# Kernel optimization log

Hardware: AMD Instinct MI355X
Metric: run time of the kernel (lower is better)

The kernel has to match this reference:

```python
import jax, jax.numpy as jnp
import numpy as np

BLOCK_H = 32
BLOCK_W = 32
HEADS = 16
SEQ = 1024
BATCH = 8
HEAD_DIM = 64


def _block_mask(mask):
    # conv with all-ones kernel, stride = block size, grouped per head == block sum-pool, then >0
    H, S, Sw = mask.shape
    nb_h, nb_w = S // BLOCK_H, Sw // BLOCK_W
    pooled = mask.reshape(H, nb_h, BLOCK_H, nb_w, BLOCK_W).sum(axis=(2, 4))
    return pooled > 0  # [H, nb_h, nb_w] bool


def setup_inputs() -> dict:
    key = jax.random.key(0)
    kq, kk, kv, km = jax.random.split(key, 4)
    q = jax.random.normal(kq, (BATCH, HEADS, SEQ, HEAD_DIM), dtype=jnp.float32)
    k = jax.random.normal(kk, (BATCH, HEADS, SEQ, HEAD_DIM), dtype=jnp.float32)
    v = jax.random.normal(kv, (BATCH, HEADS, SEQ, HEAD_DIM), dtype=jnp.float32)
    # with diagonal blocks always present (valid causal layout, matches triton usage).
    nb = SEQ // BLOCK_H
    bm = jax.random.uniform(km, (HEADS, nb, nb)) < 0.25
    bm = bm | jnp.eye(nb, dtype=bool)[None, :, :]
    # expand block mask to element-level float mask [H, S, S]
    mask = jnp.broadcast_to(
        bm[:, :, None, :, None], (HEADS, nb, BLOCK_H, nb, BLOCK_W)
    ).reshape(HEADS, SEQ, SEQ).astype(jnp.float32)
    return {"query": q, "key": k, "value": v, "mask": mask}


def reference(query, key, value, mask):
    scale = 1.0
    bm = _block_mask(mask)  # [H, nb, nb]
    nb = bm.shape[-1]
    # expand block layout back to element granularity (triton masks per-block only)
    elem = jnp.broadcast_to(
        bm[:, :, None, :, None], (bm.shape[0], nb, BLOCK_H, nb, BLOCK_W)
    ).reshape(bm.shape[0], nb * BLOCK_H, nb * BLOCK_W)
    causal = jnp.tril(jnp.ones((elem.shape[-2], elem.shape[-1]), dtype=bool))
    full = elem & causal[None]  # [H, S, S]
    # SDD: QK^T only on layout blocks; dense equivalent masks to -inf elsewhere
    scores = jnp.einsum("bhqd,bhkd->bhqk", query, key) * scale
    scores = jnp.where(full[None], scores, -jnp.inf)
    probs = jax.nn.softmax(scores, axis=-1)  # every row has a valid diagonal-block entry
    # DSD: sparse probs @ dense V
    out = jnp.einsum("bhqk,bhkd->bhqd", probs, value)
    return out
```

## Files before the change

### kernel.cpp

```cpp
#include <hip/hip_runtime.h>
#include <stdint.h>

typedef unsigned short u16;
typedef short bf16x8 __attribute__((ext_vector_type(8)));
typedef bf16x8 __attribute__((may_alias)) bf16x8_a;
typedef unsigned u32x2 __attribute__((ext_vector_type(2)));
typedef u32x2 __attribute__((may_alias)) u32x2_a;
typedef float f32x4 __attribute__((ext_vector_type(4)));
typedef f32x4 __attribute__((may_alias)) f32x4_a;

#define BATCH 8
#define HEADS 16
#define SEQ 1024
#define HD 64
#define NB 32
#define LOG2E 1.44269504f
#define MBIAS 46.16624128f
#define BLK 2048

__device__ unsigned g_bm[HEADS * NB];
__device__ u16 g_kb[(size_t)BATCH * HEADS * NB * BLK];
__device__ u16 g_kl[(size_t)BATCH * HEADS * NB * BLK];
__device__ u16 g_vt[(size_t)BATCH * HEADS * NB * BLK];

__device__ __forceinline__ u16 f2bf(float x) {
    unsigned u = __builtin_bit_cast(unsigned, x);
    u += 0x7fffu + ((u >> 16) & 1u);
    return (u16)(u >> 16);
}
__device__ __forceinline__ float bf2f(u16 h) {
    unsigned u = ((unsigned)h) << 16;
    return __builtin_bit_cast(float, u);
}
__device__ __forceinline__ bf16x8 pack8(float4 a, float4 b) {
    bf16x8 r;
    r[0] = (short)f2bf(a.x); r[1] = (short)f2bf(a.y);
    r[2] = (short)f2bf(a.z); r[3] = (short)f2bf(a.w);
    r[4] = (short)f2bf(b.x); r[5] = (short)f2bf(b.y);
    r[6] = (short)f2bf(b.z); r[7] = (short)f2bf(b.w);
    return r;
}
__device__ __forceinline__ bf16x8 pack8_res(float4 a, float4 b, bf16x8 hi) {
    bf16x8 r;
    r[0] = (short)f2bf(a.x - bf2f((u16)hi[0])); r[1] = (short)f2bf(a.y - bf2f((u16)hi[1]));
    r[2] = (short)f2bf(a.z - bf2f((u16)hi[2])); r[3] = (short)f2bf(a.w - bf2f((u16)hi[3]));
    r[4] = (short)f2bf(b.x - bf2f((u16)hi[4])); r[5] = (short)f2bf(b.y - bf2f((u16)hi[5]));
    r[6] = (short)f2bf(b.z - bf2f((u16)hi[6])); r[7] = (short)f2bf(b.w - bf2f((u16)hi[7]));
    return r;
}

__global__ __launch_bounds__(256) void prep_kv(const float* __restrict__ k,
                                               const float* __restrict__ v,
                                               const float* __restrict__ mask) {
    __shared__ float tile[32 * 65];
    int bid = blockIdx.x;
    int t = threadIdx.x;
    if (bid < 4096) {
        int bh = bid >> 5, j = bid & 31;
        int row = t >> 3, dg = t & 7;
        const float* s = k + ((size_t)(bh * SEQ + j * 32 + row)) * HD + dg * 8;
        float4 a = *(const float4*)(s);
        float4 b = *(const float4*)(s + 4);
        bf16x8 hi = pack8(a, b);
        bf16x8 lo = pack8_res(a, b, hi);
        int c = ((row >> 4) << 1) + (dg >> 2);
        int lane = (row & 15) + ((dg & 3) << 4);
        size_t o = ((size_t)(bh * NB + j)) * BLK + c * 512 + lane * 8;
        *(bf16x8*)(g_kb + o) = hi;
        *(bf16x8*)(g_kl + o) = lo;
        return;
    }
    if (bid < 6144) {
        int tb = bid - 4096;
        int bh = tb >> 4, kt = tb & 15;
        const float* src = v + ((size_t)(bh * SEQ + kt * 64)) * HD;
#pragma unroll
        for (int pass = 0; pass < 2; ++pass) {
#pragma unroll
            for (int p = 0; p < 2; ++p) {
                int row = p * 16 + (t >> 4);
                int col = (t & 15) * 4;
                float4 d = *(const float4*)(src + (size_t)(pass * 32 + row) * HD + col);
                float* tp = &tile[row * 65 + col];
                tp[0] = d.x; tp[1] = d.y; tp[2] = d.z; tp[3] = d.w;
            }
            __syncthreads();
            {
                int dd = t >> 2;
                int kc = (t & 3) * 8;
                u16 tmp[8];
#pragma unroll
                for (int i = 0; i < 8; ++i) tmp[i] = f2bf(tile[(kc + i) * 65 + dd]);
                int j = kt * 2 + pass;
                int c = dd >> 4;
                int lane = (dd & 15) + ((kc >> 3) << 4);
                size_t o = ((size_t)(bh * NB + j)) * BLK + c * 512 + lane * 8;
                *(uint4*)(g_vt + o) = *(const uint4*)tmp;
            }
            __syncthreads();
        }
        return;
    }
    int h = bid - 6144;
    int lane = t & 63;
#pragma unroll
    for (int kk2 = 0; kk2 < 4; ++kk2) {
        int tt = (kk2 << 8) | t;
        int i = tt >> 5, j = tt & 31;
        float mv = mask[(size_t)h * SEQ * SEQ + (size_t)(i * 32) * SEQ + (size_t)(j * 32)];
        bool pred = (j == i) || (j < i && mv != 0.0f);
        unsigned long long bal = __ballot(pred);
        if (lane == 0)  g_bm[h * NB + i] = (unsigned)(bal & 0xffffffffull);
        if (lane == 32) g_bm[h * NB + i] = (unsigned)(bal >> 32);
    }
}

__device__ __forceinline__ void load_blk(size_t kb, bf16x8 (&kh)[4], bf16x8 (&kl)[4],
                                         bf16x8 (&vf)[4]) {
#pragma unroll
    for (int c = 0; c < 4; ++c) {
        kh[c] = *(const bf16x8_a*)(const void*)(g_kb + kb + c * 512);
        kl[c] = *(const bf16x8_a*)(const void*)(g_kl + kb + c * 512);
        vf[c] = *(const bf16x8_a*)(const void*)(g_vt + kb + c * 512);
    }
}

__device__ __forceinline__ void compute_blk(int j, int i32, int qcol, int quad,
                                            const bf16x8 (&kh)[4], const bf16x8 (&kl)[4],
                                            const bf16x8 (&vf)[4],
                                            const bf16x8 (&qh)[2][2], const bf16x8 (&ql)[2][2],
                                            u16* pl, f32x4 (&oacc)[2][4], float& l0, float& l1) {
    f32x4 tt[2][2];
    __builtin_amdgcn_s_setprio(1);
#pragma unroll
    for (int kt = 0; kt < 2; ++kt)
#pragma unroll
        for (int t = 0; t < 2; ++t) {
            f32x4 acc = f32x4{0.f, 0.f, 0.f, 0.f};
            acc = __builtin_amdgcn_mfma_f32_16x16x32_bf16(kl[kt*2+0], qh[t][0], acc, 0, 0, 0);
            acc = __builtin_amdgcn_mfma_f32_16x16x32_bf16(kl[kt*2+1], qh[t][1], acc, 0, 0, 0);
            acc = __builtin_amdgcn_mfma_f32_16x16x32_bf16(kh[kt*2+0], ql[t][0], acc, 0, 0, 0);
            acc = __builtin_amdgcn_mfma_f32_16x16x32_bf16(kh[kt*2+1], ql[t][1], acc, 0, 0, 0);
            acc = __builtin_amdgcn_mfma_f32_16x16x32_bf16(kh[kt*2+0], qh[t][0], acc, 0, 0, 0);
            acc = __builtin_amdgcn_mfma_f32_16x16x32_bf16(kh[kt*2+1], qh[t][1], acc, 0, 0, 0);
            tt[kt][t] = acc;
        }
    __builtin_amdgcn_s_setprio(0);

    if (j == i32) {
#pragma unroll
        for (int kt = 0; kt < 2; ++kt)
#pragma unroll
            for (int t = 0; t < 2; ++t)
#pragma unroll
                for (int r = 0; r < 4; ++r) {
                    int key = kt * 16 + quad * 4 + r;
                    if (key > t * 16 + qcol) tt[kt][t][r] = -1e30f;
                }
    }

    u16 pb[2][8];
#pragma unroll
    for (int kt = 0; kt < 2; ++kt)
#pragma unroll
        for (int t = 0; t < 2; ++t) {
            float psum = 0.f;
#pragma unroll
            for (int r = 0; r < 4; ++r) {
                float e = exp2f(tt[kt][t][r] * LOG2E - MBIAS);
                u16 eb = f2bf(e);
                pb[t][kt * 4 + r] = eb;
                psum += bf2f(eb);
            }
            if (t == 0) l0 += psum; else l1 += psum;
        }

#pragma unroll
    for (int t = 0; t < 2; ++t)
#pragma unroll
        for (int kt = 0; kt < 2; ++kt) {
            u32x2 pw;
            pw[0] = (unsigned)pb[t][kt*4+0] | ((unsigned)pb[t][kt*4+1] << 16);
            pw[1] = (unsigned)pb[t][kt*4+2] | ((unsigned)pb[t][kt*4+3] << 16);
            *(u32x2_a*)(pl + (t * 16 + qcol) * 40 + kt * 16 + quad * 4) = pw;
        }
    bf16x8 pf0 = *(const bf16x8_a*)(pl + qcol * 40 + quad * 8);
    bf16x8 pf1 = *(const bf16x8_a*)(pl + (16 + qcol) * 40 + quad * 8);

    __builtin_amdgcn_s_setprio(1);
#pragma unroll
    for (int c = 0; c < 4; ++c) {
        oacc[0][c] = __builtin_amdgcn_mfma_f32_16x16x32_bf16(vf[c], pf0, oacc[0][c], 0, 0, 0);
        oacc[1][c] = __builtin_amdgcn_mfma_f32_16x16x32_bf16(vf[c], pf1, oacc[1][c], 0, 0, 0);
    }
    __builtin_amdgcn_s_setprio(0);
}

__global__ __launch_bounds__(64, 2) void attn(const float* __restrict__ q,
                                              float* __restrict__ out) {
    __shared__ __align__(16) char smem[8704];

    int lane = threadIdx.x & 63;
    int qcol = lane & 15;
    int quad = lane >> 4;

    int bid = blockIdx.x;
    int slot = bid & 7;
    int r = bid >> 3;
    int half = r >> 8;
    int rr = r & 255;
    int i32 = 31 - (rr >> 3);
    int bh = slot + ((((half << 3) | (rr & 7))) << 3);
    int h = bh & (HEADS - 1);

    bf16x8 qh[2][2], ql[2][2];
#pragma unroll
    for (int t = 0; t < 2; ++t) {
        const float* qb = q + ((size_t)(bh * SEQ + i32 * 32 + t * 16 + qcol)) * HD + quad * 8;
#pragma unroll
        for (int dh = 0; dh < 2; ++dh) {
            float4 a = *(const float4*)(qb + dh * 32);
            float4 b = *(const float4*)(qb + dh * 32 + 4);
            qh[t][dh] = pack8(a, b);
            ql[t][dh] = pack8_res(a, b, qh[t][dh]);
        }
    }

    unsigned bits = g_bm[h * NB + i32];
    size_t bhbase = (size_t)bh * NB * BLK + lane * 8;
    u16* pl = (u16*)smem;

    f32x4 oacc[2][4];
#pragma unroll
    for (int t = 0; t < 2; ++t)
#pragma unroll
        for (int c = 0; c < 4; ++c) oacc[t][c] = f32x4{0.f, 0.f, 0.f, 0.f};
    float l0 = 0.f, l1 = 0.f;

    bf16x8 khA[4], klA[4], vfA[4], khB[4], klB[4], vfB[4];
    unsigned rem = bits;
    if (rem) {
        int jA = __builtin_ctz(rem); rem &= rem - 1;
        load_blk(bhbase + (size_t)jA * BLK, khA, klA, vfA);
        for (;;) {
            int jB = -1;
            if (rem) { jB = __builtin_ctz(rem); rem &= rem - 1;
                       load_blk(bhbase + (size_t)jB * BLK, khB, klB, vfB); }
            compute_blk(jA, i32, qcol, quad, khA, klA, vfA, qh, ql, pl, oacc, l0, l1);
            if (jB < 0) break;
            jA = -1;
            if (rem) { jA = __builtin_ctz(rem); rem &= rem - 1;
                       load_blk(bhbase + (size_t)jA * BLK, khA, klA, vfA); }
            compute_blk(jB, i32, qcol, quad, khB, klB, vfB, qh, ql, pl, oacc, l0, l1);
            if (jA < 0) break;
        }
    }

    l0 += __shfl_xor(l0, 16); l0 += __shfl_xor(l0, 32);
    l1 += __shfl_xor(l1, 16); l1 += __shfl_xor(l1, 32);
    float inv[2] = {1.0f / l0, 1.0f / l1};

    float* ol = (float*)smem;
#pragma unroll
    for (int t = 0; t < 2; ++t)
#pragma unroll
        for (int c = 0; c < 4; ++c) {
            f32x4 val;
            val[0] = oacc[t][c][0] * inv[t]; val[1] = oacc[t][c][1] * inv[t];
            val[2] = oacc[t][c][2] * inv[t]; val[3] = oacc[t][c][3] * inv[t];
            *(f32x4_a*)(ol + (t * 16 + qcol) * 68 + c * 16 + quad * 4) = val;
        }
    float* obase = out + ((size_t)(bh * SEQ + i32 * 32)) * HD;
#pragma unroll
    for (int gr = 0; gr < 8; ++gr) {
        int row = gr * 4 + (lane >> 4);
        int colf = (lane & 15) * 4;
        f32x4 val = *(const f32x4_a*)(ol + row * 68 + colf);
        *(float4*)(obase + (size_t)row * HD + colf) = make_float4(val[0], val[1], val[2], val[3]);
    }
}

extern "C" void kernel_launch(void* const* d_in, const int* in_sizes, int n_in,
                              void* d_out, int out_size, void* d_ws, size_t ws_size,
                              hipStream_t stream) {
    const float* q = (const float*)d_in[0];
    const float* k = (const float*)d_in[1];
    const float* v = (const float*)d_in[2];
    const float* mask = (const float*)d_in[3];
    float* out = (float*)d_out;

    prep_kv<<<4096 + 2048 + 16, 256, 0, stream>>>(k, v, mask);
    attn<<<4096, 64, 0, stream>>>(q, out);
}
```

Before: 200.4 us.

## Split query block across two waves with shared LDS-staged K/V double buffer

The attention kernel now uses two waves per block, each owning 16 query rows, instead of one wave handling all 32 rows. K-hi, K-lo and V^T tiles are copied into a double-buffered LDS stage with global_load_lds, split between the waves, so both waves share one copy of each key block. The next block's copy is issued before the current one is computed. This cuts per-wave register pressure and duplicate global loads, and it writes output directly from registers. In exchange it adds a __syncthreads and a full vmcnt wait on every iteration.

```diff
diff --git a/kernel.cpp b/kernel.cpp
--- a/kernel.cpp
+++ b/kernel.cpp
@@ -47,6 +47,12 @@
     r[4] = (short)f2bf(b.x - bf2f((u16)hi[4])); r[5] = (short)f2bf(b.y - bf2f((u16)hi[5]));
     r[6] = (short)f2bf(b.z - bf2f((u16)hi[6])); r[7] = (short)f2bf(b.w - bf2f((u16)hi[7]));
     return r;
+}
+
+__device__ __forceinline__ void cp16(u16* lds_uniform, const u16* g_perlane) {
+    __builtin_amdgcn_global_load_lds(
+        (const __attribute__((address_space(1))) unsigned int*)g_perlane,
+        (__attribute__((address_space(3))) unsigned int*)lds_uniform, 16, 0, 0);
 }
 
 __global__ __launch_bounds__(256) void prep_kv(const float* __restrict__ k,
@@ -115,91 +121,12 @@
     }
 }
 
-__device__ __forceinline__ void load_blk(size_t kb, bf16x8 (&kh)[4], bf16x8 (&kl)[4],
-                                         bf16x8 (&vf)[4]) {
-#pragma unroll
-    for (int c = 0; c < 4; ++c) {
-        kh[c] = *(const bf16x8_a*)(const void*)(g_kb + kb + c * 512);
-        kl[c] = *(const bf16x8_a*)(const void*)(g_kl + kb + c * 512);
-        vf[c] = *(const bf16x8_a*)(const void*)(g_vt + kb + c * 512);
-    }
-}
-
-__device__ __forceinline__ void compute_blk(int j, int i32, int qcol, int quad,
-                                            const bf16x8 (&kh)[4], const bf16x8 (&kl)[4],
-                                            const bf16x8 (&vf)[4],
-                                            const bf16x8 (&qh)[2][2], const bf16x8 (&ql)[2][2],
-                                            u16* pl, f32x4 (&oacc)[2][4], float& l0, float& l1) {
-    f32x4 tt[2][2];
-    __builtin_amdgcn_s_setprio(1);
-#pragma unroll
-    for (int kt = 0; kt < 2; ++kt)
-#pragma unroll
-        for (int t = 0; t < 2; ++t) {
-            f32x4 acc = f32x4{0.f, 0.f, 0.f, 0.f};
-            acc = __builtin_amdgcn_mfma_f32_16x16x32_bf16(kl[kt*2+0], qh[t][0], acc, 0, 0, 0);
-            acc = __builtin_amdgcn_mfma_f32_16x16x32_bf16(kl[kt*2+1], qh[t][1], acc, 0, 0, 0);
-            acc = __builtin_amdgcn_mfma_f32_16x16x32_bf16(kh[kt*2+0], ql[t][0], acc, 0, 0, 0);
-            acc = __builtin_amdgcn_mfma_f32_16x16x32_bf16(kh[kt*2+1], ql[t][1], acc, 0, 0, 0);
-            acc = __builtin_amdgcn_mfma_f32_16x16x32_bf16(kh[kt*2+0], qh[t][0], acc, 0, 0, 0);
-            acc = __builtin_amdgcn_mfma_f32_16x16x32_bf16(kh[kt*2+1], qh[t][1], acc, 0, 0, 0);
-            tt[kt][t] = acc;
-        }
-    __builtin_amdgcn_s_setprio(0);
-
-    if (j == i32) {
-#pragma unroll
-        for (int kt = 0; kt < 2; ++kt)
-#pragma unroll
-            for (int t = 0; t < 2; ++t)
-#pragma unroll
-                for (int r = 0; r < 4; ++r) {
-                    int key = kt * 16 + quad * 4 + r;
-                    if (key > t * 16 + qcol) tt[kt][t][r] = -1e30f;
-                }
-    }
-
-    u16 pb[2][8];
-#pragma unroll
-    for (int kt = 0; kt < 2; ++kt)
-#pragma unroll
-        for (int t = 0; t < 2; ++t) {
-            float psum = 0.f;
-#pragma unroll
-            for (int r = 0; r < 4; ++r) {
-                float e = exp2f(tt[kt][t][r] * LOG2E - MBIAS);
-                u16 eb = f2bf(e);
-                pb[t][kt * 4 + r] = eb;
-                psum += bf2f(eb);
-            }
-            if (t == 0) l0 += psum; else l1 += psum;
-        }
-
-#pragma unroll
-    for (int t = 0; t < 2; ++t)
-#pragma unroll
-        for (int kt = 0; kt < 2; ++kt) {
-            u32x2 pw;
-            pw[0] = (unsigned)pb[t][kt*4+0] | ((unsigned)pb[t][kt*4+1] << 16);
-            pw[1] = (unsigned)pb[t][kt*4+2] | ((unsigned)pb[t][kt*4+3] << 16);
-            *(u32x2_a*)(pl + (t * 16 + qcol) * 40 + kt * 16 + quad * 4) = pw;
-        }
-    bf16x8 pf0 = *(const bf16x8_a*)(pl + qcol * 40 + quad * 8);
-    bf16x8 pf1 = *(const bf16x8_a*)(pl + (16 + qcol) * 40 + quad * 8);
-
-    __builtin_amdgcn_s_setprio(1);
-#pragma unroll
-    for (int c = 0; c < 4; ++c) {
-        oacc[0][c] = __builtin_amdgcn_mfma_f32_16x16x32_bf16(vf[c], pf0, oacc[0][c], 0, 0, 0);
-        oacc[1][c] = __builtin_amdgcn_mfma_f32_16x16x32_bf16(vf[c], pf1, oacc[1][c], 0, 0, 0);
-    }
-    __builtin_amdgcn_s_setprio(0);
-}
-
-__global__ __launch_bounds__(64, 2) void attn(const float* __restrict__ q,
-                                              float* __restrict__ out) {
-    __shared__ __align__(16) char smem[8704];
-
+__global__ __launch_bounds__(128) void attn(const float* __restrict__ q,
+                                            float* __restrict__ out) {
+    __shared__ __align__(16) u16 stage[2][3][2048];
+    __shared__ __align__(16) u16 pbuf[2][640];
+
+    int w = threadIdx.x >> 6;
     int lane = threadIdx.x & 63;
     int qcol = lane & 15;
     int quad = lane >> 4;
@@ -213,70 +140,130 @@
     int bh = slot + ((((half << 3) | (rr & 7))) << 3);
     int h = bh & (HEADS - 1);
 
-    bf16x8 qh[2][2], ql[2][2];
-#pragma unroll
-    for (int t = 0; t < 2; ++t) {
-        const float* qb = q + ((size_t)(bh * SEQ + i32 * 32 + t * 16 + qcol)) * HD + quad * 8;
+    bf16x8 qh[2], ql[2];
+    {
+        const float* qb = q + ((size_t)(bh * SEQ + i32 * 32 + w * 16 + qcol)) * HD + quad * 8;
 #pragma unroll
         for (int dh = 0; dh < 2; ++dh) {
             float4 a = *(const float4*)(qb + dh * 32);
             float4 b = *(const float4*)(qb + dh * 32 + 4);
-            qh[t][dh] = pack8(a, b);
-            ql[t][dh] = pack8_res(a, b, qh[t][dh]);
+            qh[dh] = pack8(a, b);
+            ql[dh] = pack8_res(a, b, qh[dh]);
         }
     }
 
     unsigned bits = g_bm[h * NB + i32];
     size_t bhbase = (size_t)bh * NB * BLK + lane * 8;
-    u16* pl = (u16*)smem;
-
-    f32x4 oacc[2][4];
-#pragma unroll
-    for (int t = 0; t < 2; ++t)
-#pragma unroll
-        for (int c = 0; c < 4; ++c) oacc[t][c] = f32x4{0.f, 0.f, 0.f, 0.f};
-    float l0 = 0.f, l1 = 0.f;
-
-    bf16x8 khA[4], klA[4], vfA[4], khB[4], klB[4], vfB[4];
+    u16* pl = pbuf[w];
+
+    f32x4 oacc[4];
+#pragma unroll
+    for (int c = 0; c < 4; ++c) oacc[c] = f32x4{0.f, 0.f, 0.f, 0.f};
+    float lsum = 0.f;
+
+    auto STAGE = [&](int buf, int j) {
+        size_t base = bhbase + (size_t)j * BLK;
+        if (w == 0) {
+#pragma unroll
+            for (int c = 0; c < 4; ++c) cp16(&stage[buf][0][c * 512], g_kb + base + c * 512);
+#pragma unroll
+            for (int c = 0; c < 2; ++c) cp16(&stage[buf][1][c * 512], g_kl + base + c * 512);
+        } else {
+#pragma unroll
+            for (int c = 2; c < 4; ++c) cp16(&stage[buf][1][c * 512], g_kl + base + c * 512);
+#pragma unroll
+            for (int c = 0; c < 4; ++c) cp16(&stage[buf][2][c * 512], g_vt + base + c * 512);
+        }
+    };
+
     unsigned rem = bits;
-    if (rem) {
-        int jA = __builtin_ctz(rem); rem &= rem - 1;
-        load_blk(bhbase + (size_t)jA * BLK, khA, klA, vfA);
-        for (;;) {
-            int jB = -1;
-            if (rem) { jB = __builtin_ctz(rem); rem &= rem - 1;
-                       load_blk(bhbase + (size_t)jB * BLK, khB, klB, vfB); }
-            compute_blk(jA, i32, qcol, quad, khA, klA, vfA, qh, ql, pl, oacc, l0, l1);
-            if (jB < 0) break;
-            jA = -1;
-            if (rem) { jA = __builtin_ctz(rem); rem &= rem - 1;
-                       load_blk(bhbase + (size_t)jA * BLK, khA, klA, vfA); }
-            compute_blk(jB, i32, qcol, quad, khB, klB, vfB, qh, ql, pl, oacc, l0, l1);
-            if (jA < 0) break;
-        }
-    }
-
-    l0 += __shfl_xor(l0, 16); l0 += __shfl_xor(l0, 32);
-    l1 += __shfl_xor(l1, 16); l1 += __shfl_xor(l1, 32);
-    float inv[2] = {1.0f / l0, 1.0f / l1};
-
-    float* ol = (float*)smem;
-#pragma unroll
-    for (int t = 0; t < 2; ++t)
+    int jcur = __builtin_ctz(rem); rem &= rem - 1;
+    STAGE(0, jcur);
+    asm volatile("s_waitcnt vmcnt(0)" ::: "memory");
+    __syncthreads();
+
+    int buf = 0;
+    for (;;) {
+        int jn = -1;
+        if (rem) { jn = __builtin_ctz(rem); rem &= rem - 1; STAGE(buf ^ 1, jn); }
+
+        bf16x8 kh[4], kl[4], vf[4];
 #pragma unroll
         for (int c = 0; c < 4; ++c) {
-            f32x4 val;
-            val[0] = oacc[t][c][0] * inv[t]; val[1] = oacc[t][c][1] * inv[t];
-            val[2] = oacc[t][c][2] * inv[t]; val[3] = oacc[t][c][3] * inv[t];
-            *(f32x4_a*)(ol + (t * 16 + qcol) * 68 + c * 16 + quad * 4) = val;
-        }
-    float* obase = out + ((size_t)(bh * SEQ + i32 * 32)) * HD;
-#pragma unroll
-    for (int gr = 0; gr < 8; ++gr) {
-        int row = gr * 4 + (lane >> 4);
-        int colf = (lane & 15) * 4;
-        f32x4 val = *(const f32x4_a*)(ol + row * 68 + colf);
-        *(float4*)(obase + (size_t)row * HD + colf) = make_float4(val[0], val[1], val[2], val[3]);
+            kh[c] = *(const bf16x8_a*)(&stage[buf][0][c * 512 + lane * 8]);
+            kl[c] = *(const bf16x8_a*)(&stage[buf][1][c * 512 + lane * 8]);
+            vf[c] = *(const bf16x8_a*)(&stage[buf][2][c * 512 + lane * 8]);
+        }
+
+        f32x4 tt[2];
+        __builtin_amdgcn_s_setprio(1);
+#pragma unroll
+        for (int kt = 0; kt < 2; ++kt) {
+            f32x4 acc = f32x4{0.f, 0.f, 0.f, 0.f};
+            acc = __builtin_amdgcn_mfma_f32_16x16x32_bf16(kl[kt*2+0], qh[0], acc, 0, 0, 0);
+            acc = __builtin_amdgcn_mfma_f32_16x16x32_bf16(kl[kt*2+1], qh[1], acc, 0, 0, 0);
+            acc = __builtin_amdgcn_mfma_f32_16x16x32_bf16(kh[kt*2+0], ql[0], acc, 0, 0, 0);
+            acc = __builtin_amdgcn_mfma_f32_16x16x32_bf16(kh[kt*2+1], ql[1], acc, 0, 0, 0);
+            acc = __builtin_amdgcn_mfma_f32_16x16x32_bf16(kh[kt*2+0], qh[0], acc, 0, 0, 0);
+            acc = __builtin_amdgcn_mfma_f32_16x16x32_bf16(kh[kt*2+1], qh[1], acc, 0, 0, 0);
+            tt[kt] = acc;
+        }
+        __builtin_amdgcn_s_setprio(0);
+
+        if (jcur == i32) {
+#pragma unroll
+            for (int kt = 0; kt < 2; ++kt)
+#pragma unroll
+                for (int rr2 = 0; rr2 < 4; ++rr2) {
+                    int key = kt * 16 + quad * 4 + rr2;
+                    if (key > w * 16 + qcol) tt[kt][rr2] = -1e30f;
+                }
+        }
+
+        u16 pb[8];
+#pragma unroll
+        for (int kt = 0; kt < 2; ++kt) {
+            float psum = 0.f;
+#pragma unroll
+            for (int rr2 = 0; rr2 < 4; ++rr2) {
+                float e = exp2f(tt[kt][rr2] * LOG2E - MBIAS);
+                u16 eb = f2bf(e);
+                pb[kt * 4 + rr2] = eb;
+                psum += bf2f(eb);
+            }
+            lsum += psum;
+        }
+
+#pragma unroll
+        for (int kt = 0; kt < 2; ++kt) {
+            u32x2 pw;
+            pw[0] = (unsigned)pb[kt*4+0] | ((unsigned)pb[kt*4+1] << 16);
+            pw[1] = (unsigned)pb[kt*4+2] | ((unsigned)pb[kt*4+3] << 16);
+            *(u32x2_a*)(pl + qcol * 40 + kt * 16 + quad * 4) = pw;
+        }
+        bf16x8 pf = *(const bf16x8_a*)(pl + qcol * 40 + quad * 8);
+
+        __builtin_amdgcn_s_setprio(1);
+#pragma unroll
+        for (int c = 0; c < 4; ++c)
+            oacc[c] = __builtin_amdgcn_mfma_f32_16x16x32_bf16(vf[c], pf, oacc[c], 0, 0, 0);
+        __builtin_amdgcn_s_setprio(0);
+
+        asm volatile("s_waitcnt vmcnt(0)" ::: "memory");
+        __syncthreads();
+        if (jn < 0) break;
+        jcur = jn; buf ^= 1;
+    }
+
+    lsum += __shfl_xor(lsum, 16); lsum += __shfl_xor(lsum, 32);
+    float inv = 1.0f / lsum;
+
+    float* ob = out + ((size_t)(bh * SEQ + i32 * 32 + w * 16 + qcol)) * HD + quad * 4;
+#pragma unroll
+    for (int c = 0; c < 4; ++c) {
+        float4 val = make_float4(oacc[c][0] * inv, oacc[c][1] * inv,
+                                 oacc[c][2] * inv, oacc[c][3] * inv);
+        *(float4*)(ob + c * 16) = val;
     }
 }
 
@@ -290,5 +277,5 @@
     float* out = (float*)d_out;
 
     prep_kv<<<4096 + 2048 + 16, 256, 0, stream>>>(k, v, mask);
-    attn<<<4096, 64, 0, stream>>>(q, out);
-}
+    attn<<<4096, 128, 0, stream>>>(q, out);
+}
```

After: 203.7 us. Within noise of the previous version (+1.6%).
